# Performance work log

Measured on AMD Instinct MI355X. Metric: run time of the kernel, lower is better.

## Reference

```python
import jax, jax.numpy as jnp
import numpy as np

B, S, V, E, H, C = 64, 512, 32000, 512, 1024, 2


def _init_linear(key, fan_in, fan_out):
    kw, kb = jax.random.split(key)
    bound = 1.0 / np.sqrt(fan_in)
    w = jax.random.uniform(kw, (fan_in, fan_out), jnp.float32, -bound, bound)
    b = jax.random.uniform(kb, (fan_out,), jnp.float32, -bound, bound)
    return w, b


def setup_inputs() -> dict:
    key = jax.random.key(0)
    ks = jax.random.split(key, 16)
    inp = {"x": jax.random.randint(ks[0], (B, S), 0, V, dtype=jnp.int64),
           "emb": jax.random.normal(ks[1], (V, E), jnp.float32) * 0.02}
    # per-direction, per-layer RNN cell params (layer0: E->H, layer1: H->H)
    names = [("fw0", E), ("fw1", H), ("bw0", E), ("bw1", H)]
    for i, (nm, fin) in enumerate(names):
        wih, bih = _init_linear(ks[2 + 2 * i], fin, H)
        whh, bhh = _init_linear(ks[3 + 2 * i], H, H)
        inp[nm + "_wih"], inp[nm + "_bih"] = wih, bih
        inp[nm + "_whh"], inp[nm + "_bhh"] = whh, bhh
    inp["fc1_w"], inp["fc1_b"] = _init_linear(ks[10], 2 * H, 64)
    inp["fc2_w"], inp["fc2_b"] = _init_linear(ks[11], 64, C)
    return inp


def _run_direction(seq, p0, p1):
    # seq: [S, B, E]; stacked 2-layer tanh RNN; layer l at step t consumes
    # layer l-1's output at the SAME step t (matches the torch inner loop).
    b = seq.shape[1]
    h_dim = p0[2].shape[0]
    init = (jnp.zeros((b, h_dim), seq.dtype), jnp.zeros((b, h_dim), seq.dtype))

    def step(carry, xt):
        h0, h1 = carry
        h0 = jnp.tanh(xt @ p0[0] + p0[1] + h0 @ p0[2] + p0[3])
        h1 = jnp.tanh(h0 @ p1[0] + p1[1] + h1 @ p1[2] + p1[3])
        return (h0, h1), None

    (h0, h1), _ = jax.lax.scan(step, init, seq)
    return h1  # final hidden of top layer


def reference(x, emb, fw0_wih, fw0_bih, fw0_whh, fw0_bhh,
              fw1_wih, fw1_bih, fw1_whh, fw1_bhh,
              bw0_wih, bw0_bih, bw0_whh, bw0_bhh,
              bw1_wih, bw1_bih, bw1_whh, bw1_bhh,
              fc1_w, fc1_b, fc2_w, fc2_b):
    embed_x = jnp.transpose(emb[x], (1, 0, 2))  # [S, B, E]
    h_fwd = _run_direction(embed_x,
                           (fw0_wih, fw0_bih, fw0_whh, fw0_bhh),
                           (fw1_wih, fw1_bih, fw1_whh, fw1_bhh))
    h_bwd = _run_direction(embed_x[::-1],
                           (bw0_wih, bw0_bih, bw0_whh, bw0_bhh),
                           (bw1_wih, bw1_bih, bw1_whh, bw1_bhh))
    hidden = jnp.concatenate([h_fwd, h_bwd], axis=1)  # [B, 2H]
    return (hidden @ fc1_w + fc1_b) @ fc2_w + fc2_b  # [B, C]
```

## Files before the change

### kernel.cpp

```cpp
#include <hip/hip_runtime.h>
#include <hip/hip_bf16.h>
#include <hip/hip_fp16.h>

#define SS 512
#define BB 64
#define EE 512
#define HH 1024

typedef _Float16 f16x8 __attribute__((ext_vector_type(8)));
typedef _Float16 f16x4 __attribute__((ext_vector_type(4)));
typedef float f32x4 __attribute__((ext_vector_type(4)));
typedef unsigned long long u64;

__device__ __forceinline__ f16x8 ldh8(const _Float16* p) {
    return *reinterpret_cast<const f16x8*>(p);
}

__global__ void prep_wt(const float* __restrict__ wih, const float* __restrict__ whh,
                        int K1, int K, _Float16* __restrict__ out)
{
    int k = blockIdx.x;
    const float* src = (k < K1) ? (wih + (size_t)k * HH) : (whh + (size_t)(k - K1) * HH);
    for (int n = threadIdx.x; n < HH; n += blockDim.x)
        out[(size_t)n * K + k] = (_Float16)src[n];
}

__global__ void prep_bias(const float* f0ih, const float* f0hh,
                          const float* f1ih, const float* f1hh,
                          const float* b0ih, const float* b0hh,
                          const float* b1ih, const float* b1hh,
                          float* __restrict__ bias)
{
    int i = threadIdx.x;
    bias[i]          = f0ih[i] + f0hh[i];
    bias[1024 + i]   = f1ih[i] + f1hh[i];
    bias[2048 + i]   = b0ih[i] + b0hh[i];
    bias[3072 + i]   = b1ih[i] + b1hh[i];
}

__global__ void prep_embx(const int* __restrict__ x, const float* __restrict__ emb,
                          _Float16* __restrict__ embx)
{
    int t = blockIdx.x >> 6, b = blockIdx.x & 63;
    const float* src = emb + (size_t)x[b * SS + t] * EE;
    _Float16* dst = embx + ((size_t)t * BB + b) * EE;
    int i = threadIdx.x * 4;
    float4 v = *reinterpret_cast<const float4*>(src + i);
    f16x4 h;
    h[0] = (_Float16)v.x; h[1] = (_Float16)v.y;
    h[2] = (_Float16)v.z; h[3] = (_Float16)v.w;
    *reinterpret_cast<f16x4*>(dst + i) = h;
}

__device__ __forceinline__ f16x8 ld_tile(const u64* __restrict__ slot, int k0, int m, int kg, int r)
{
    union { u64 u[2]; f16x8 v; } z;
    const u64* p = slot + ((k0 >> 5) * 512 + m * 128 + kg * 32 + r * 2);
    z.u[0] = __hip_atomic_load(p,     __ATOMIC_RELAXED, __HIP_MEMORY_SCOPE_AGENT);
    z.u[1] = __hip_atomic_load(p + 1, __ATOMIC_RELAXED, __HIP_MEMORY_SCOPE_AGENT);
    return z.v;
}

__device__ __forceinline__ void st_tile(u64* __restrict__ slot, int row, int col4, f16x4 hv)
{
    union { u64 u; f16x4 v; } z; z.v = hv;
    u64* p = slot + ((col4 >> 5) * 512 + (row >> 4) * 128 + ((col4 >> 3) & 3) * 32
                     + (row & 15) * 2 + ((col4 >> 2) & 1));
    __hip_atomic_store(p, z.u, __ATOMIC_RELAXED, __HIP_MEMORY_SCOPE_AGENT);
}

__device__ __forceinline__ void wave_wait(const unsigned* a , unsigned ta,
                                          const unsigned* b , unsigned tb)
{
    const int lane = threadIdx.x & 63;
    const unsigned* pa = a + (lane & 15) * 16;
    const unsigned* pb = b ? b + lane * 16 : nullptr;
    for (;;) {
        bool ok = __hip_atomic_load(pa, __ATOMIC_RELAXED, __HIP_MEMORY_SCOPE_AGENT) >= ta;
        if (pb)
            ok &= __hip_atomic_load(pb, __ATOMIC_RELAXED, __HIP_MEMORY_SCOPE_AGENT) >= tb;
        if (__all(ok)) break;
        __builtin_amdgcn_s_sleep(1);
    }
}

__global__ __launch_bounds__(256, 1)
void rnn_persistent(const int* __restrict__ x, const float* __restrict__ emb,
                    const _Float16* __restrict__ embx,
                    const _Float16* __restrict__ W0f, const _Float16* __restrict__ W1f,
                    const _Float16* __restrict__ W0b, const _Float16* __restrict__ W1b,
                    const float* __restrict__ bias,
                    u64* __restrict__ h0f, u64* __restrict__ h1f,
                    u64* __restrict__ h0b, u64* __restrict__ h1b,
                    float* __restrict__ h1fin, unsigned* __restrict__ flg)
{
    const int bid  = blockIdx.x;
    const int task = bid >> 6;
    const int tile = bid & 63;
    const int dir  = task & 1;
    const bool isL1 = task >= 2;
    const int lane = threadIdx.x & 63;
    const int wave = threadIdx.x >> 6;
    const int r    = lane & 15;
    const int kg   = lane >> 4;
    const int tid  = threadIdx.x;

    const int K  = isL1 ? 2048 : 1536;
    const int Kp = K + 26;

    __shared__ _Float16 Wlds[16 * 2074];
    __shared__ float red[4][64][20];

    {
        const _Float16* Wg = isL1 ? (dir ? W1b : W1f) : (dir ? W0b : W0f);
        int rowlen = K >> 3;
        for (int idx = tid; idx < 16 * rowlen; idx += 256) {
            int row = idx / rowlen, kk = (idx - row * rowlen) * 8;
            f16x8 v = ldh8(Wg + (size_t)(tile * 16 + row) * K + kk);
            *reinterpret_cast<f16x8*>(&Wlds[row * Kp + kk]) = v;
        }
    }
    __syncthreads();

    u64* hbuf0 = dir ? h0b : h0f;
    u64* h1buf = dir ? h1b : h1f;

    unsigned* F_L0 = flg + (size_t)dir * 64 * 16;
    unsigned* F_L1 = flg + (size_t)(2 + dir) * 64 * 16;
    unsigned* F_own = (isL1 ? F_L1 : F_L0) + tile * 16;
    const unsigned* myslice_L0 = F_L0 + 16 * wave * 16;
    const unsigned* myslice_L1 = F_L1 + 16 * wave * 16;

    for (int t = 0; t < SS; ++t) {
        f32x4 acc[4];
#pragma unroll
        for (int m = 0; m < 4; ++m) acc[m] = (f32x4){0.f, 0.f, 0.f, 0.f};

        if (!isL1) {
            const int t_eff = dir ? (SS - 1 - t) : t;
            if (embx) {
                const _Float16* Aemb = embx + (size_t)t_eff * (BB * EE);
#pragma unroll
                for (int i = 0; i < 4; ++i) {
                    const int k = wave * 128 + i * 32;
                    f16x8 bf = *reinterpret_cast<const f16x8*>(&Wlds[r * Kp + k + kg * 8]);
#pragma unroll
                    for (int m = 0; m < 4; ++m) {
                        f16x8 a = ldh8(Aemb + (m * 16 + r) * EE + k + kg * 8);
                        acc[m] = __builtin_amdgcn_mfma_f32_16x16x32_f16(a, bf, acc[m], 0, 0, 0);
                    }
                }
            } else {
                const float* erow[4];
#pragma unroll
                for (int m = 0; m < 4; ++m)
                    erow[m] = emb + (size_t)x[(m * 16 + r) * SS + t_eff] * EE;
#pragma unroll
                for (int i = 0; i < 4; ++i) {
                    const int k = wave * 128 + i * 32;
                    f16x8 bf = *reinterpret_cast<const f16x8*>(&Wlds[r * Kp + k + kg * 8]);
#pragma unroll
                    for (int m = 0; m < 4; ++m) {
                        const float* p = erow[m] + k + kg * 8;
                        float4 lo = *reinterpret_cast<const float4*>(p);
                        float4 hi = *reinterpret_cast<const float4*>(p + 4);
                        f16x8 a;
                        a[0] = (_Float16)lo.x; a[1] = (_Float16)lo.y;
                        a[2] = (_Float16)lo.z; a[3] = (_Float16)lo.w;
                        a[4] = (_Float16)hi.x; a[5] = (_Float16)hi.y;
                        a[6] = (_Float16)hi.z; a[7] = (_Float16)hi.w;
                        acc[m] = __builtin_amdgcn_mfma_f32_16x16x32_f16(a, bf, acc[m], 0, 0, 0);
                    }
                }
            }
            if (t >= 1) {
                wave_wait(myslice_L0, (unsigned)t,
                          (t >= 4) ? F_L1 : nullptr, (unsigned)(t - 3));
                const u64* hprev = hbuf0 + (size_t)((t - 1) & 3) * 16384;
#pragma unroll
                for (int i = 0; i < 8; ++i) {
                    const int k = wave * 256 + i * 32;
                    f16x8 bf = *reinterpret_cast<const f16x8*>(&Wlds[r * Kp + EE + k + kg * 8]);
#pragma unroll
                    for (int m = 0; m < 4; ++m) {
                        f16x8 a = ld_tile(hprev, k, m, kg, r);
                        acc[m] = __builtin_amdgcn_mfma_f32_16x16x32_f16(a, bf, acc[m], 0, 0, 0);
                    }
                }
            }
        } else {
            if (t >= 1) {
                wave_wait(myslice_L1, (unsigned)t, nullptr, 0u);
                const u64* h1prev = h1buf + (size_t)((t - 1) & 3) * 16384;
#pragma unroll
                for (int i = 0; i < 8; ++i) {
                    const int k = wave * 256 + i * 32;
                    f16x8 bf = *reinterpret_cast<const f16x8*>(&Wlds[r * Kp + HH + k + kg * 8]);
#pragma unroll
                    for (int m = 0; m < 4; ++m) {
                        f16x8 a = ld_tile(h1prev, k, m, kg, r);
                        acc[m] = __builtin_amdgcn_mfma_f32_16x16x32_f16(a, bf, acc[m], 0, 0, 0);
                    }
                }
            }
            wave_wait(myslice_L0, (unsigned)(t + 1), nullptr, 0u);
            const u64* h0cur = hbuf0 + (size_t)(t & 3) * 16384;
#pragma unroll
            for (int i = 0; i < 8; ++i) {
                const int k = wave * 256 + i * 32;
                f16x8 bf = *reinterpret_cast<const f16x8*>(&Wlds[r * Kp + k + kg * 8]);
#pragma unroll
                for (int m = 0; m < 4; ++m) {
                    f16x8 a = ld_tile(h0cur, k, m, kg, r);
                    acc[m] = __builtin_amdgcn_mfma_f32_16x16x32_f16(a, bf, acc[m], 0, 0, 0);
                }
            }
        }

#pragma unroll
        for (int m = 0; m < 4; ++m)
#pragma unroll
            for (int rr = 0; rr < 4; ++rr)
                red[wave][m * 16 + kg * 4 + rr][r] = acc[m][rr];
        __syncthreads();
        {
            const int row = tid >> 2;
            const int c   = (tid & 3) * 4;
            f32x4 s = *reinterpret_cast<f32x4*>(&red[0][row][c]);
#pragma unroll
            for (int w = 1; w < 4; ++w) s += *reinterpret_cast<f32x4*>(&red[w][row][c]);
            const int nb = tile * 16 + c;
            const float* bp = bias + (isL1 ? 1024 : 0) + (dir ? 2048 : 0) + nb;
            float4 bv = *reinterpret_cast<const float4*>(bp);
            float v0 = tanhf(s[0] + bv.x), v1 = tanhf(s[1] + bv.y);
            float v2 = tanhf(s[2] + bv.z), v3 = tanhf(s[3] + bv.w);
            f16x4 hv; hv[0] = (_Float16)v0; hv[1] = (_Float16)v1;
            hv[2] = (_Float16)v2; hv[3] = (_Float16)v3;
            u64* hout = (isL1 ? h1buf : hbuf0) + (size_t)(t & 3) * 16384;
            st_tile(hout, row, nb, hv);
            if (isL1 && t == SS - 1) {
                float4 fv; fv.x = v0; fv.y = v1; fv.z = v2; fv.w = v3;
                *reinterpret_cast<float4*>(h1fin + (size_t)dir * (BB * HH) + row * HH + nb) = fv;
            }
        }
        __syncthreads();
        if (tid == 0)
            __hip_atomic_store(F_own, (unsigned)(t + 1), __ATOMIC_RELAXED,
                               __HIP_MEMORY_SCOPE_AGENT);
    }
}

__global__ void fc1_kernel(const float* __restrict__ h1fin, const float* __restrict__ w,
                           const float* __restrict__ b, float* __restrict__ v)
{
    int idx = blockIdx.x * 256 + threadIdx.x;
    int bb = idx >> 6, nn = idx & 63;
    const float* hf = h1fin + bb * HH;
    const float* hb = h1fin + BB * HH + bb * HH;
    float s = b[nn];
#pragma unroll 8
    for (int k = 0; k < HH; ++k) s += hf[k] * w[k * 64 + nn];
#pragma unroll 8
    for (int k = 0; k < HH; ++k) s += hb[k] * w[(HH + k) * 64 + nn];
    v[idx] = s;
}

__global__ void fc2_kernel(const float* __restrict__ v, const float* __restrict__ w,
                           const float* __restrict__ b, float* __restrict__ out)
{
    int idx = threadIdx.x;
    if (idx >= BB * 2) return;
    int bb = idx >> 1, c = idx & 1;
    float s = b[c];
    const float* vb = v + bb * 64;
#pragma unroll
    for (int j = 0; j < 64; ++j) s += vb[j] * w[j * 2 + c];
    out[bb * 2 + c] = s;
}

extern "C" void kernel_launch(void* const* d_in, const int* in_sizes, int n_in,
                              void* d_out, int out_size, void* d_ws, size_t ws_size,
                              hipStream_t stream)
{
    const int*   x        = (const int*)  d_in[0];
    const float* emb      = (const float*)d_in[1];
    const float* fw0_wih  = (const float*)d_in[2];
    const float* fw0_bih  = (const float*)d_in[3];
    const float* fw0_whh  = (const float*)d_in[4];
    const float* fw0_bhh  = (const float*)d_in[5];
    const float* fw1_wih  = (const float*)d_in[6];
    const float* fw1_bih  = (const float*)d_in[7];
    const float* fw1_whh  = (const float*)d_in[8];
    const float* fw1_bhh  = (const float*)d_in[9];
    const float* bw0_wih  = (const float*)d_in[10];
    const float* bw0_bih  = (const float*)d_in[11];
    const float* bw0_whh  = (const float*)d_in[12];
    const float* bw0_bhh  = (const float*)d_in[13];
    const float* bw1_wih  = (const float*)d_in[14];
    const float* bw1_bih  = (const float*)d_in[15];
    const float* bw1_whh  = (const float*)d_in[16];
    const float* bw1_bhh  = (const float*)d_in[17];
    const float* fc1_w    = (const float*)d_in[18];
    const float* fc1_b    = (const float*)d_in[19];
    const float* fc2_w    = (const float*)d_in[20];
    const float* fc2_b    = (const float*)d_in[21];

    size_t off = 0;
    char* wsb = (char*)d_ws;
    auto take = [&](size_t bytes) -> void* {
        void* p = wsb + off;
        off += (bytes + 255) & ~(size_t)255;
        return p;
    };
    _Float16* W0f   = (_Float16*)take((size_t)HH * 1536 * 2);
    _Float16* W1f   = (_Float16*)take((size_t)HH * 2048 * 2);
    _Float16* W0b   = (_Float16*)take((size_t)HH * 1536 * 2);
    _Float16* W1b   = (_Float16*)take((size_t)HH * 2048 * 2);
    float*    bias  = (float*)   take(4096 * 4);
    u64*      h0f   = (u64*)     take((size_t)4 * 16384 * 8);
    u64*      h1f   = (u64*)     take((size_t)4 * 16384 * 8);
    u64*      h0b   = (u64*)     take((size_t)4 * 16384 * 8);
    u64*      h1b   = (u64*)     take((size_t)4 * 16384 * 8);
    float*    h1fin = (float*)   take((size_t)2 * BB * HH * 4);
    float*    vmid  = (float*)   take(4096 * 4);
    unsigned* flg   = (unsigned*)take((size_t)4 * 64 * 16 * 4);
    _Float16* embx  = (_Float16*)take((size_t)SS * BB * EE * 2);
    bool use_embx = (ws_size >= off);

    prep_wt<<<1536, 256, 0, stream>>>(fw0_wih, fw0_whh, EE, 1536, W0f);
    prep_wt<<<2048, 256, 0, stream>>>(fw1_wih, fw1_whh, HH, 2048, W1f);
    prep_wt<<<1536, 256, 0, stream>>>(bw0_wih, bw0_whh, EE, 1536, W0b);
    prep_wt<<<2048, 256, 0, stream>>>(bw1_wih, bw1_whh, HH, 2048, W1b);
    prep_bias<<<1, 1024, 0, stream>>>(fw0_bih, fw0_bhh, fw1_bih, fw1_bhh,
                                      bw0_bih, bw0_bhh, bw1_bih, bw1_bhh, bias);
    if (use_embx)
        prep_embx<<<SS * BB, 128, 0, stream>>>(x, emb, embx);
    hipMemsetAsync(flg, 0, (size_t)4 * 64 * 16 * 4, stream);

    const _Float16* embx_arg = use_embx ? embx : nullptr;
    void* args[] = {(void*)&x, (void*)&emb, (void*)&embx_arg,
                    (void*)&W0f, (void*)&W1f, (void*)&W0b, (void*)&W1b,
                    (void*)&bias, (void*)&h0f, (void*)&h1f, (void*)&h0b, (void*)&h1b,
                    (void*)&h1fin, (void*)&flg};
    hipLaunchCooperativeKernel((void*)rnn_persistent, dim3(256), dim3(256), args, 0, stream);

    fc1_kernel<<<16, 256, 0, stream>>>(h1fin, fc1_w, fc1_b, vmid);
    fc2_kernel<<<1, 128, 0, stream>>>(vmid, fc2_w, fc2_b, (float*)d_out);
}
```

Measured before the change: 4.370 ms.

## Fuse both RNN layers per block with register-resident weights and skewed pipeline

The persistent kernel drops from 256 blocks (separate layer-0 and layer-1 tasks) to 128 blocks. Each block computes layer 0 at step t and layer 1 at step t-1 in one skewed loop, so every step needs only one flag wait and one block barrier. Weights are pre-swizzled into MFMA fragment order and held in registers instead of LDS, and the embedding input is stored in fragment order for coalesced loads. The aim is to halve the cross-block synchronisation points and remove LDS weight reads. The cost is heavy register pressure and half as many CUs doing the per-step work.

```diff
diff --git a/kernel.cpp b/kernel.cpp
--- a/kernel.cpp
+++ b/kernel.cpp
@@ -19,10 +19,20 @@
 __global__ void prep_wt(const float* __restrict__ wih, const float* __restrict__ whh,
                         int K1, int K, _Float16* __restrict__ out)
 {
-    int k = blockIdx.x;
-    const float* src = (k < K1) ? (wih + (size_t)k * HH) : (whh + (size_t)(k - K1) * HH);
-    for (int n = threadIdx.x; n < HH; n += blockDim.x)
-        out[(size_t)n * K + k] = (_Float16)src[n];
+    int tile = blockIdx.x;
+    int nv = 2 * K;
+    for (int v = threadIdx.x; v < nv; v += blockDim.x) {
+        int chunk = v >> 6, kg = (v >> 4) & 3, rr = v & 15;
+        int n = tile * 16 + rr;
+        f16x8 o;
+#pragma unroll
+        for (int j = 0; j < 8; ++j) {
+            int k = chunk * 32 + kg * 8 + j;
+            float s = (k < K1) ? wih[(size_t)k * HH + n] : whh[(size_t)(k - K1) * HH + n];
+            o[j] = (_Float16)s;
+        }
+        *reinterpret_cast<f16x8*>(out + ((size_t)tile * nv + v) * 8) = o;
+    }
 }
 
 __global__ void prep_bias(const float* f0ih, const float* f0hh,
@@ -43,19 +53,21 @@
 {
     int t = blockIdx.x >> 6, b = blockIdx.x & 63;
     const float* src = emb + (size_t)x[b * SS + t] * EE;
-    _Float16* dst = embx + ((size_t)t * BB + b) * EE;
-    int i = threadIdx.x * 4;
-    float4 v = *reinterpret_cast<const float4*>(src + i);
-    f16x4 h;
-    h[0] = (_Float16)v.x; h[1] = (_Float16)v.y;
-    h[2] = (_Float16)v.z; h[3] = (_Float16)v.w;
-    *reinterpret_cast<f16x4*>(dst + i) = h;
-}
-
-__device__ __forceinline__ f16x8 ld_tile(const u64* __restrict__ slot, int k0, int m, int kg, int r)
+    int m = b >> 4, rr = b & 15;
+    int e0 = threadIdx.x * 8;
+    int chunk = e0 >> 5, kg = (e0 >> 3) & 3;
+    float4 lo = *reinterpret_cast<const float4*>(src + e0);
+    float4 hi = *reinterpret_cast<const float4*>(src + e0 + 4);
+    f16x8 h;
+    h[0] = (_Float16)lo.x; h[1] = (_Float16)lo.y; h[2] = (_Float16)lo.z; h[3] = (_Float16)lo.w;
+    h[4] = (_Float16)hi.x; h[5] = (_Float16)hi.y; h[6] = (_Float16)hi.z; h[7] = (_Float16)hi.w;
+    *reinterpret_cast<f16x8*>(embx + (size_t)t * (BB * EE)
+                              + (((size_t)chunk * 4 + m) * 64 + kg * 16 + rr) * 8) = h;
+}
+
+__device__ __forceinline__ f16x8 ld_frag(const u64* __restrict__ p)
 {
     union { u64 u[2]; f16x8 v; } z;
-    const u64* p = slot + ((k0 >> 5) * 512 + m * 128 + kg * 32 + r * 2);
     z.u[0] = __hip_atomic_load(p,     __ATOMIC_RELAXED, __HIP_MEMORY_SCOPE_AGENT);
     z.u[1] = __hip_atomic_load(p + 1, __ATOMIC_RELAXED, __HIP_MEMORY_SCOPE_AGENT);
     return z.v;
@@ -64,24 +76,9 @@
 __device__ __forceinline__ void st_tile(u64* __restrict__ slot, int row, int col4, f16x4 hv)
 {
     union { u64 u; f16x4 v; } z; z.v = hv;
-    u64* p = slot + ((col4 >> 5) * 512 + (row >> 4) * 128 + ((col4 >> 3) & 3) * 32
-                     + (row & 15) * 2 + ((col4 >> 2) & 1));
+    u64* p = slot + ((col4 >> 5) * 512 + (row >> 4) * 128
+                     + (((col4 >> 3) & 3) * 16 + (row & 15)) * 2 + ((col4 >> 2) & 1));
     __hip_atomic_store(p, z.u, __ATOMIC_RELAXED, __HIP_MEMORY_SCOPE_AGENT);
-}
-
-__device__ __forceinline__ void wave_wait(const unsigned* a , unsigned ta,
-                                          const unsigned* b , unsigned tb)
-{
-    const int lane = threadIdx.x & 63;
-    const unsigned* pa = a + (lane & 15) * 16;
-    const unsigned* pb = b ? b + lane * 16 : nullptr;
-    for (;;) {
-        bool ok = __hip_atomic_load(pa, __ATOMIC_RELAXED, __HIP_MEMORY_SCOPE_AGENT) >= ta;
-        if (pb)
-            ok &= __hip_atomic_load(pb, __ATOMIC_RELAXED, __HIP_MEMORY_SCOPE_AGENT) >= tb;
-        if (__all(ok)) break;
-        __builtin_amdgcn_s_sleep(1);
-    }
 }
 
 __global__ __launch_bounds__(256, 1)
@@ -95,59 +92,61 @@
                     float* __restrict__ h1fin, unsigned* __restrict__ flg)
 {
     const int bid  = blockIdx.x;
-    const int task = bid >> 6;
+    const int dir  = bid >> 6;
     const int tile = bid & 63;
-    const int dir  = task & 1;
-    const bool isL1 = task >= 2;
-    const int lane = threadIdx.x & 63;
-    const int wave = threadIdx.x >> 6;
+    const int tid  = threadIdx.x;
+    const int lane = tid & 63;
+    const int wave = tid >> 6;
     const int r    = lane & 15;
     const int kg   = lane >> 4;
-    const int tid  = threadIdx.x;
-
-    const int K  = isL1 ? 2048 : 1536;
-    const int Kp = K + 26;
-
-    __shared__ _Float16 Wlds[16 * 2074];
-    __shared__ float red[4][64][20];
-
-    {
-        const _Float16* Wg = isL1 ? (dir ? W1b : W1f) : (dir ? W0b : W0f);
-        int rowlen = K >> 3;
-        for (int idx = tid; idx < 16 * rowlen; idx += 256) {
-            int row = idx / rowlen, kk = (idx - row * rowlen) * 8;
-            f16x8 v = ldh8(Wg + (size_t)(tile * 16 + row) * K + kk);
-            *reinterpret_cast<f16x8*>(&Wlds[row * Kp + kk]) = v;
-        }
+    const int c0   = wave * 8;
+
+    __shared__ float red[4][64][40];
+
+    const _Float16* W0g = (dir ? W0b : W0f) + (size_t)tile * (2 * 1536 * 8);
+    const _Float16* W1g = (dir ? W1b : W1f) + (size_t)tile * (2 * 2048 * 8);
+    f16x8 w0e[4], w0h[8], w1a[8], w1b[8];
+#pragma unroll
+    for (int i = 0; i < 4; ++i)
+        w0e[i] = ldh8(W0g + ((size_t)(wave * 4 + i) * 64 + lane) * 8);
+#pragma unroll
+    for (int i = 0; i < 8; ++i) {
+        w0h[i] = ldh8(W0g + ((size_t)(16 + c0 + i) * 64 + lane) * 8);
+        w1a[i] = ldh8(W1g + ((size_t)(c0 + i) * 64 + lane) * 8);
+        w1b[i] = ldh8(W1g + ((size_t)(32 + c0 + i) * 64 + lane) * 8);
     }
-    __syncthreads();
 
     u64* hbuf0 = dir ? h0b : h0f;
-    u64* h1buf = dir ? h1b : h1f;
-
-    unsigned* F_L0 = flg + (size_t)dir * 64 * 16;
-    unsigned* F_L1 = flg + (size_t)(2 + dir) * 64 * 16;
-    unsigned* F_own = (isL1 ? F_L1 : F_L0) + tile * 16;
-    const unsigned* myslice_L0 = F_L0 + 16 * wave * 16;
-    const unsigned* myslice_L1 = F_L1 + 16 * wave * 16;
-
-    for (int t = 0; t < SS; ++t) {
-        f32x4 acc[4];
-#pragma unroll
-        for (int m = 0; m < 4; ++m) acc[m] = (f32x4){0.f, 0.f, 0.f, 0.f};
-
-        if (!isL1) {
+    u64* hbuf1 = dir ? h1b : h1f;
+
+    unsigned* F_own = flg + ((size_t)dir * 64 + tile) * 16;
+    const unsigned* myflag = flg + (((size_t)dir * 64 + wave * 16 + (lane & 15))) * 16;
+
+    const int erow_ = tid >> 2;
+    const int ec    = (tid & 3) * 4;
+    const int nb    = tile * 16 + ec;
+    const float4 bv0 = *reinterpret_cast<const float4*>(bias + (dir ? 2048 : 0) + nb);
+    const float4 bv1 = *reinterpret_cast<const float4*>(bias + 1024 + (dir ? 2048 : 0) + nb);
+
+    for (int t = 0; t <= SS; ++t) {
+        f32x4 acc0[4], acc1[4];
+#pragma unroll
+        for (int m = 0; m < 4; ++m) {
+            acc0[m] = (f32x4){0.f, 0.f, 0.f, 0.f};
+            acc1[m] = (f32x4){0.f, 0.f, 0.f, 0.f};
+        }
+
+        if (t < SS) {
             const int t_eff = dir ? (SS - 1 - t) : t;
             if (embx) {
-                const _Float16* Aemb = embx + (size_t)t_eff * (BB * EE);
+                const _Float16* Ae = embx + (size_t)t_eff * (BB * EE);
 #pragma unroll
                 for (int i = 0; i < 4; ++i) {
-                    const int k = wave * 128 + i * 32;
-                    f16x8 bf = *reinterpret_cast<const f16x8*>(&Wlds[r * Kp + k + kg * 8]);
+                    const int ch = wave * 4 + i;
 #pragma unroll
                     for (int m = 0; m < 4; ++m) {
-                        f16x8 a = ldh8(Aemb + (m * 16 + r) * EE + k + kg * 8);
-                        acc[m] = __builtin_amdgcn_mfma_f32_16x16x32_f16(a, bf, acc[m], 0, 0, 0);
+                        f16x8 a = ldh8(Ae + (((size_t)ch * 4 + m) * 64 + lane) * 8);
+                        acc0[m] = __builtin_amdgcn_mfma_f32_16x16x32_f16(a, w0e[i], acc0[m], 0, 0, 0);
                     }
                 }
             } else {
@@ -157,11 +156,10 @@
                     erow[m] = emb + (size_t)x[(m * 16 + r) * SS + t_eff] * EE;
 #pragma unroll
                 for (int i = 0; i < 4; ++i) {
-                    const int k = wave * 128 + i * 32;
-                    f16x8 bf = *reinterpret_cast<const f16x8*>(&Wlds[r * Kp + k + kg * 8]);
+                    const int k = (wave * 4 + i) * 32 + kg * 8;
 #pragma unroll
                     for (int m = 0; m < 4; ++m) {
-                        const float* p = erow[m] + k + kg * 8;
+                        const float* p = erow[m] + k;
                         float4 lo = *reinterpret_cast<const float4*>(p);
                         float4 hi = *reinterpret_cast<const float4*>(p + 4);
                         f16x8 a;
@@ -169,78 +167,82 @@
                         a[2] = (_Float16)lo.z; a[3] = (_Float16)lo.w;
                         a[4] = (_Float16)hi.x; a[5] = (_Float16)hi.y;
                         a[6] = (_Float16)hi.z; a[7] = (_Float16)hi.w;
-                        acc[m] = __builtin_amdgcn_mfma_f32_16x16x32_f16(a, bf, acc[m], 0, 0, 0);
+                        acc0[m] = __builtin_amdgcn_mfma_f32_16x16x32_f16(a, w0e[i], acc0[m], 0, 0, 0);
                     }
                 }
             }
-            if (t >= 1) {
-                wave_wait(myslice_L0, (unsigned)t,
-                          (t >= 4) ? F_L1 : nullptr, (unsigned)(t - 3));
-                const u64* hprev = hbuf0 + (size_t)((t - 1) & 3) * 16384;
-#pragma unroll
-                for (int i = 0; i < 8; ++i) {
-                    const int k = wave * 256 + i * 32;
-                    f16x8 bf = *reinterpret_cast<const f16x8*>(&Wlds[r * Kp + EE + k + kg * 8]);
-#pragma unroll
-                    for (int m = 0; m < 4; ++m) {
-                        f16x8 a = ld_tile(hprev, k, m, kg, r);
-                        acc[m] = __builtin_amdgcn_mfma_f32_16x16x32_f16(a, bf, acc[m], 0, 0, 0);
-                    }
+        }
+
+        if (t >= 1) {
+            while (!__all(__hip_atomic_load(myflag, __ATOMIC_RELAXED,
+                                            __HIP_MEMORY_SCOPE_AGENT) >= (unsigned)t))
+                __builtin_amdgcn_s_sleep(1);
+
+            const u64* h0p = hbuf0 + (size_t)((t - 1) & 3) * 16384;
+            f16x8 h0a[8][4];
+#pragma unroll
+            for (int i = 0; i < 8; ++i)
+#pragma unroll
+                for (int m = 0; m < 4; ++m)
+                    h0a[i][m] = ld_frag(h0p + (size_t)(c0 + i) * 512 + m * 128 + lane * 2);
+#pragma unroll
+            for (int i = 0; i < 8; ++i)
+#pragma unroll
+                for (int m = 0; m < 4; ++m) {
+                    acc0[m] = __builtin_amdgcn_mfma_f32_16x16x32_f16(h0a[i][m], w0h[i], acc0[m], 0, 0, 0);
+                    acc1[m] = __builtin_amdgcn_mfma_f32_16x16x32_f16(h0a[i][m], w1a[i], acc1[m], 0, 0, 0);
                 }
-            }
-        } else {
-            if (t >= 1) {
-                wave_wait(myslice_L1, (unsigned)t, nullptr, 0u);
-                const u64* h1prev = h1buf + (size_t)((t - 1) & 3) * 16384;
-#pragma unroll
-                for (int i = 0; i < 8; ++i) {
-                    const int k = wave * 256 + i * 32;
-                    f16x8 bf = *reinterpret_cast<const f16x8*>(&Wlds[r * Kp + HH + k + kg * 8]);
-#pragma unroll
-                    for (int m = 0; m < 4; ++m) {
-                        f16x8 a = ld_tile(h1prev, k, m, kg, r);
-                        acc[m] = __builtin_amdgcn_mfma_f32_16x16x32_f16(a, bf, acc[m], 0, 0, 0);
-                    }
-                }
-            }
-            wave_wait(myslice_L0, (unsigned)(t + 1), nullptr, 0u);
-            const u64* h0cur = hbuf0 + (size_t)(t & 3) * 16384;
-#pragma unroll
-            for (int i = 0; i < 8; ++i) {
-                const int k = wave * 256 + i * 32;
-                f16x8 bf = *reinterpret_cast<const f16x8*>(&Wlds[r * Kp + k + kg * 8]);
-#pragma unroll
-                for (int m = 0; m < 4; ++m) {
-                    f16x8 a = ld_tile(h0cur, k, m, kg, r);
-                    acc[m] = __builtin_amdgcn_mfma_f32_16x16x32_f16(a, bf, acc[m], 0, 0, 0);
-                }
+
+            if (t >= 2) {
+                const u64* h1p = hbuf1 + (size_t)((t - 2) & 3) * 16384;
+                f16x8 h1a[8][4];
+#pragma unroll
+                for (int i = 0; i < 8; ++i)
+#pragma unroll
+                    for (int m = 0; m < 4; ++m)
+                        h1a[i][m] = ld_frag(h1p + (size_t)(c0 + i) * 512 + m * 128 + lane * 2);
+#pragma unroll
+                for (int i = 0; i < 8; ++i)
+#pragma unroll
+                    for (int m = 0; m < 4; ++m)
+                        acc1[m] = __builtin_amdgcn_mfma_f32_16x16x32_f16(h1a[i][m], w1b[i], acc1[m], 0, 0, 0);
             }
         }
 
 #pragma unroll
         for (int m = 0; m < 4; ++m)
 #pragma unroll
-            for (int rr = 0; rr < 4; ++rr)
-                red[wave][m * 16 + kg * 4 + rr][r] = acc[m][rr];
+            for (int q = 0; q < 4; ++q) {
+                red[wave][m * 16 + kg * 4 + q][r]      = acc0[m][q];
+                red[wave][m * 16 + kg * 4 + q][20 + r] = acc1[m][q];
+            }
         __syncthreads();
         {
-            const int row = tid >> 2;
-            const int c   = (tid & 3) * 4;
-            f32x4 s = *reinterpret_cast<f32x4*>(&red[0][row][c]);
-#pragma unroll
-            for (int w = 1; w < 4; ++w) s += *reinterpret_cast<f32x4*>(&red[w][row][c]);
-            const int nb = tile * 16 + c;
-            const float* bp = bias + (isL1 ? 1024 : 0) + (dir ? 2048 : 0) + nb;
-            float4 bv = *reinterpret_cast<const float4*>(bp);
-            float v0 = tanhf(s[0] + bv.x), v1 = tanhf(s[1] + bv.y);
-            float v2 = tanhf(s[2] + bv.z), v3 = tanhf(s[3] + bv.w);
-            f16x4 hv; hv[0] = (_Float16)v0; hv[1] = (_Float16)v1;
-            hv[2] = (_Float16)v2; hv[3] = (_Float16)v3;
-            u64* hout = (isL1 ? h1buf : hbuf0) + (size_t)(t & 3) * 16384;
-            st_tile(hout, row, nb, hv);
-            if (isL1 && t == SS - 1) {
-                float4 fv; fv.x = v0; fv.y = v1; fv.z = v2; fv.w = v3;
-                *reinterpret_cast<float4*>(h1fin + (size_t)dir * (BB * HH) + row * HH + nb) = fv;
+            f32x4 s0 = *reinterpret_cast<f32x4*>(&red[0][erow_][ec]);
+            f32x4 s1 = *reinterpret_cast<f32x4*>(&red[0][erow_][20 + ec]);
+#pragma unroll
+            for (int w = 1; w < 4; ++w) {
+                s0 += *reinterpret_cast<f32x4*>(&red[w][erow_][ec]);
+                s1 += *reinterpret_cast<f32x4*>(&red[w][erow_][20 + ec]);
+            }
+            if (t < SS) {
+                float v0 = tanhf(s0[0] + bv0.x), v1 = tanhf(s0[1] + bv0.y);
+                float v2 = tanhf(s0[2] + bv0.z), v3 = tanhf(s0[3] + bv0.w);
+                f16x4 hv; hv[0] = (_Float16)v0; hv[1] = (_Float16)v1;
+                hv[2] = (_Float16)v2; hv[3] = (_Float16)v3;
+                st_tile(hbuf0 + (size_t)(t & 3) * 16384, erow_, nb, hv);
+            }
+            if (t >= 1) {
+                float v0 = tanhf(s1[0] + bv1.x), v1 = tanhf(s1[1] + bv1.y);
+                float v2 = tanhf(s1[2] + bv1.z), v3 = tanhf(s1[3] + bv1.w);
+                f16x4 hv; hv[0] = (_Float16)v0; hv[1] = (_Float16)v1;
+                hv[2] = (_Float16)v2; hv[3] = (_Float16)v3;
+                st_tile(hbuf1 + (size_t)((t - 1) & 3) * 16384, erow_, nb, hv);
+                if (t == SS) {
+                    float4 fv; fv.x = v0; fv.y = v1; fv.z = v2; fv.w = v3;
+                    *reinterpret_cast<float4*>(h1fin + (size_t)dir * (BB * HH)
+                                               + (size_t)erow_ * HH + nb) = fv;
+                }
             }
         }
         __syncthreads();
@@ -312,10 +314,10 @@
         off += (bytes + 255) & ~(size_t)255;
         return p;
     };
-    _Float16* W0f   = (_Float16*)take((size_t)HH * 1536 * 2);
-    _Float16* W1f   = (_Float16*)take((size_t)HH * 2048 * 2);
-    _Float16* W0b   = (_Float16*)take((size_t)HH * 1536 * 2);
-    _Float16* W1b   = (_Float16*)take((size_t)HH * 2048 * 2);
+    _Float16* W0f   = (_Float16*)take((size_t)1024 * 1536 * 2);
+    _Float16* W1f   = (_Float16*)take((size_t)1024 * 2048 * 2);
+    _Float16* W0b   = (_Float16*)take((size_t)1024 * 1536 * 2);
+    _Float16* W1b   = (_Float16*)take((size_t)1024 * 2048 * 2);
     float*    bias  = (float*)   take(4096 * 4);
     u64*      h0f   = (u64*)     take((size_t)4 * 16384 * 8);
     u64*      h1f   = (u64*)     take((size_t)4 * 16384 * 8);
@@ -323,26 +325,26 @@
     u64*      h1b   = (u64*)     take((size_t)4 * 16384 * 8);
     float*    h1fin = (float*)   take((size_t)2 * BB * HH * 4);
     float*    vmid  = (float*)   take(4096 * 4);
-    unsigned* flg   = (unsigned*)take((size_t)4 * 64 * 16 * 4);
+    unsigned* flg   = (unsigned*)take((size_t)128 * 16 * 4);
     _Float16* embx  = (_Float16*)take((size_t)SS * BB * EE * 2);
     bool use_embx = (ws_size >= off);
 
-    prep_wt<<<1536, 256, 0, stream>>>(fw0_wih, fw0_whh, EE, 1536, W0f);
-    prep_wt<<<2048, 256, 0, stream>>>(fw1_wih, fw1_whh, HH, 2048, W1f);
-    prep_wt<<<1536, 256, 0, stream>>>(bw0_wih, bw0_whh, EE, 1536, W0b);
-    prep_wt<<<2048, 256, 0, stream>>>(bw1_wih, bw1_whh, HH, 2048, W1b);
+    prep_wt<<<64, 256, 0, stream>>>(fw0_wih, fw0_whh, EE, 1536, W0f);
+    prep_wt<<<64, 256, 0, stream>>>(fw1_wih, fw1_whh, HH, 2048, W1f);
+    prep_wt<<<64, 256, 0, stream>>>(bw0_wih, bw0_whh, EE, 1536, W0b);
+    prep_wt<<<64, 256, 0, stream>>>(bw1_wih, bw1_whh, HH, 2048, W1b);
     prep_bias<<<1, 1024, 0, stream>>>(fw0_bih, fw0_bhh, fw1_bih, fw1_bhh,
                                       bw0_bih, bw0_bhh, bw1_bih, bw1_bhh, bias);
     if (use_embx)
-        prep_embx<<<SS * BB, 128, 0, stream>>>(x, emb, embx);
-    hipMemsetAsync(flg, 0, (size_t)4 * 64 * 16 * 4, stream);
+        prep_embx<<<SS * BB, 64, 0, stream>>>(x, emb, embx);
+    hipMemsetAsync(flg, 0, (size_t)128 * 16 * 4, stream);
 
     const _Float16* embx_arg = use_embx ? embx : nullptr;
     void* args[] = {(void*)&x, (void*)&emb, (void*)&embx_arg,
                     (void*)&W0f, (void*)&W1f, (void*)&W0b, (void*)&W1b,
                     (void*)&bias, (void*)&h0f, (void*)&h1f, (void*)&h0b, (void*)&h1b,
                     (void*)&h1fin, (void*)&flg};
-    hipLaunchCooperativeKernel((void*)rnn_persistent, dim3(256), dim3(256), args, 0, stream);
+    hipLaunchCooperativeKernel((void*)rnn_persistent, dim3(128), dim3(256), args, 0, stream);
 
     fc1_kernel<<<16, 256, 0, stream>>>(h1fin, fc1_w, fc1_b, vmid);
     fc2_kernel<<<1, 128, 0, stream>>>(vmid, fc2_w, fc2_b, (float*)d_out);
```

Result: slower. 6.388 ms (+46.2%).
